# Performance work log

Measured on AMD Instinct MI355X. Metric: run time of the kernel, lower is better.

Reference implementation:

```python
import jax, jax.numpy as jnp
import numpy as np

B, C, H, W = 16, 128, 64, 64
L, ND = 512, 256
GROUPS = 32
EPS = 1e-6


def setup_inputs() -> dict:
    key = jax.random.key(0)
    ks = jax.random.split(key, 8)
    return {
        "x": jax.random.normal(ks[0], (B, C, H, W), dtype=jnp.float32),
        "nd": jax.random.normal(ks[1], (B, L, ND), dtype=jnp.float32),
        "gn_gamma": jnp.ones((C,), dtype=jnp.float32),
        "gn_beta": jnp.zeros((C,), dtype=jnp.float32),
        "q_w": jax.random.normal(ks[2], (C, C), dtype=jnp.float32) * 0.02,
        "q_b": jax.random.normal(ks[3], (C,), dtype=jnp.float32) * 0.02,
        "nd_w": jax.random.normal(ks[4], (C, ND), dtype=jnp.float32) * 0.02,
        "nd_b": jax.random.normal(ks[5], (C,), dtype=jnp.float32) * 0.02,
        "proj_w": jax.random.normal(ks[6], (C, C), dtype=jnp.float32) * 0.02,
        "proj_b": jax.random.normal(ks[7], (C,), dtype=jnp.float32) * 0.02,
    }


def _group_norm(x, gamma, beta):
    b, c, h, w = x.shape
    xr = x.reshape(b, GROUPS, c // GROUPS, h, w)
    mean = xr.mean(axis=(2, 3, 4), keepdims=True)
    var = xr.var(axis=(2, 3, 4), keepdims=True)
    xn = ((xr - mean) * jax.lax.rsqrt(var + EPS)).reshape(b, c, h, w)
    return xn * gamma[None, :, None, None] + beta[None, :, None, None]


def reference(x, nd, gn_gamma, gn_beta, q_w, q_b, nd_w, nd_b, proj_w, proj_b):
    b, c, h, w = x.shape
    hn = _group_norm(x, gn_gamma, gn_beta)
    # 1x1 conv query -> [b, hw, c]
    q = jnp.einsum('bchw,oc->bhwo', hn, q_w).reshape(b, h * w, c) + q_b
    # silu + linear projection of conditioning; k and v use identical projection/input
    kv = jax.nn.silu(nd) @ nd_w.T + nd_b  # [b, L, c]
    # attention: [b, hw, L]
    logits = jnp.einsum('bnc,blc->bnl', q, kv) * (c ** -0.5)
    attn = jax.nn.softmax(logits, axis=2)
    # weighted sum of v -> [b, c, hw] -> [b, c, h, w]
    out = jnp.einsum('blc,bnl->bcn', kv, attn).reshape(b, c, h, w)
    # 1x1 conv projection
    out = jnp.einsum('bchw,oc->bohw', out, proj_w) + proj_b[None, :, None, None]
    return x + out
```

## Files before the change

### kernel.cpp

```cpp
#include <hip/hip_runtime.h>
#include <math.h>

constexpr int kB = 16, kC = 128, kHW = 4096, kL = 512, kND = 256, kG = 32;
constexpr float kEps = 1e-6f;
constexpr float kScale = 0.08838834764831845f;

typedef short sv8 __attribute__((ext_vector_type(8)));
typedef int   iv4 __attribute__((ext_vector_type(4)));
typedef float f32x16 __attribute__((ext_vector_type(16)));

static __device__ __forceinline__ unsigned short f2bf(float f) {
    unsigned int u = __builtin_bit_cast(unsigned int, f);
    u += 0x7fffu + ((u >> 16) & 1u);
    return (unsigned short)(u >> 16);
}
static __device__ __forceinline__ float bf2f(unsigned short s) {
    unsigned int u = ((unsigned int)s) << 16;
    return __builtin_bit_cast(float, u);
}
static __device__ __forceinline__ unsigned int pack2(float a, float b) {
    return (unsigned int)f2bf(a) | ((unsigned int)f2bf(b) << 16);
}

#define GLOAD_LDS16(gp, lp)                                                     \
    __builtin_amdgcn_global_load_lds(                                           \
        (const __attribute__((address_space(1))) void*)(gp),                    \
        (__attribute__((address_space(3))) void*)(lp), 16, 0, 0)

__global__ __launch_bounds__(256) void prep_all_k(
    const float* __restrict__ x, const float* __restrict__ nd,
    const float* __restrict__ nd_w, const float* __restrict__ nd_b,
    const float* __restrict__ proj_w, const float* __restrict__ q_w,
    const float* __restrict__ gamma, const float* __restrict__ beta,
    float* __restrict__ gab, unsigned short* __restrict__ kv_bf,
    unsigned short* __restrict__ kvT_bf, unsigned short* __restrict__ pwb,
    unsigned short* __restrict__ qwb)
{
    __shared__ float s_lds[8][256];
    __shared__ float w_lds[128][68];
    __shared__ float t_lds[8][129];
    __shared__ float red8[8];
    const int bid = blockIdx.x;
    const int tid = threadIdx.x;

    if (bid < 512) {
        const float4* p4 = (const float4*)(x + (size_t)bid * 4 * kHW);
        float s = 0.f, ss = 0.f;
        for (int i = tid; i < 4096; i += 256) {
            float4 v = p4[i];
            s  += (v.x + v.y) + (v.z + v.w);
            ss += (v.x * v.x + v.y * v.y) + (v.z * v.z + v.w * v.w);
        }
#pragma unroll
        for (int off = 1; off < 64; off <<= 1) {
            s  += __shfl_xor(s, off, 64);
            ss += __shfl_xor(ss, off, 64);
        }
        int wid = tid >> 6;
        if ((tid & 63) == 0) { red8[wid] = s; red8[wid + 4] = ss; }
        __syncthreads();
        if (tid == 0) {
            float S  = (red8[0] + red8[1]) + (red8[2] + red8[3]);
            float SS = (red8[4] + red8[5]) + (red8[6] + red8[7]);
            float mean = S * (1.f / 16384.f);
            float var  = SS * (1.f / 16384.f) - mean * mean;
            red8[0] = mean;
            red8[1] = rsqrtf(var + kEps);
        }
        __syncthreads();
        if (tid < 4) {
            int bb = bid >> 5, g = bid & 31, c = g * 4 + tid;
            float mean = red8[0], rstd = red8[1];
            float ga = gamma[c] * rstd;
            gab[bb * 256 + c]       = ga;
            gab[bb * 256 + 128 + c] = beta[c] - mean * ga;
        }
        return;
    }
    if (bid >= 1536) {
        const float* src = (bid < 1552) ? proj_w : q_w;
        unsigned short* dst = (bid < 1552) ? pwb : qwb;
        int i = (((bid - 1536) & 15) * 256 + tid) * 4;
        float4 v = *(const float4*)(src + i);
        dst[i + 0] = f2bf(v.x); dst[i + 1] = f2bf(v.y);
        dst[i + 2] = f2bf(v.z); dst[i + 3] = f2bf(v.w);
        return;
    }
    {
        int idx0 = bid - 512;
        int b = idx0 >> 6;
        int l0 = (idx0 & 63) * 8;
        const float4* ndp = (const float4*)(nd + ((size_t)b * kL + l0) * kND);
#pragma unroll
        for (int r = 0; r < 2; r++) {
            int idx = tid + r * 256;
            int row = idx >> 6;
            int c4 = idx & 63;
            float4 v = ndp[row * 64 + c4];
            v.x = v.x / (1.f + __expf(-v.x));
            v.y = v.y / (1.f + __expf(-v.y));
            v.z = v.z / (1.f + __expf(-v.z));
            v.w = v.w / (1.f + __expf(-v.w));
            *(float4*)&s_lds[row][c4 * 4] = v;
        }
        float acc[4] = {0.f, 0.f, 0.f, 0.f};
        int lr = tid >> 5;
        int oq = tid & 31;
        for (int d0 = 0; d0 < kND; d0 += 64) {
            __syncthreads();
#pragma unroll
            for (int r = 0; r < 8; r++) {
                int idx = tid + r * 256;
                int row = idx >> 4;
                int c4 = idx & 15;
                float4 v = ((const float4*)(nd_w + (size_t)row * kND + d0))[c4];
                *(float4*)&w_lds[row][c4 * 4] = v;
            }
            __syncthreads();
            for (int dd = 0; dd < 64; dd += 4) {
                float4 sv = *(const float4*)&s_lds[lr][d0 + dd];
#pragma unroll
                for (int j = 0; j < 4; j++) {
                    float4 wv = *(const float4*)&w_lds[oq + 32 * j][dd];
                    acc[j] += sv.x * wv.x + sv.y * wv.y + sv.z * wv.z + sv.w * wv.w;
                }
            }
        }
#pragma unroll
        for (int j = 0; j < 4; j++) {
            int o = oq + 32 * j;
            float vout = acc[j] + nd_b[o];
            kv_bf[((size_t)b * kL + l0 + lr) * kC + o] = f2bf(vout);
            t_lds[lr][o] = vout;
        }
        __syncthreads();
        int o = tid >> 1, lh = (tid & 1) * 4;
        unsigned long long pk = 0;
#pragma unroll
        for (int i = 0; i < 4; i++)
            pk |= (unsigned long long)f2bf(t_lds[lh + i][o]) << (16 * i);
        *(unsigned long long*)(kvT_bf + ((size_t)b * kC + o) * kL + l0 + lh) = pk;
    }
}

__global__ __launch_bounds__(256, 2) void attn_k(
    const float* __restrict__ x,
    const float* __restrict__ gab,
    const float* __restrict__ q_b,
    const unsigned short* __restrict__ qwb,
    const unsigned short* __restrict__ kvb,
    const unsigned short* __restrict__ kvtb,
    const unsigned short* __restrict__ pwb,
    const float* __restrict__ proj_b,
    float* __restrict__ out)
{
    __shared__ __align__(16) char smem[51200];

    const int flat = blockIdx.y * gridDim.x + blockIdx.x;
    const int b  = ((flat & 7) << 1) | ((flat >> 3) & 1);
    const int n0 = (flat >> 4) * 128;
    const int tid = threadIdx.x;
    const int wave = tid >> 6;
    const int lane = tid & 63;
    const int lrow = lane & 31;
    const int hi = lane >> 5;
    const int swzA = (lrow & 15) << 4;
    const int swzT = ((lrow >> 1) & 3) << 4;

    float* x_lds = (float*)(smem + 32768);
    float* gtab  = (float*)(smem + 49152);

    const unsigned short* kvB  = kvb  + (size_t)b * kL * kC;
    const unsigned short* kvtB = kvtb + (size_t)b * kC * kL;

#define STAGE_TILE(tt) do {                                                     \
        int l0s = (tt) << 5;                                                    \
        char* dA = smem + (((tt) & 1) * 8192);                                  \
        char* dT = smem + 16384 + (((tt) & 1) * 8192);                          \
        _Pragma("unroll")                                                       \
        for (int i = 0; i < 2; i++) {                                           \
            int l = i * 16 + wave * 4 + (lane >> 4);                            \
            int ch = lane & 15;                                                 \
            const unsigned short* gs =                                          \
                kvB + (size_t)(l0s + l) * kC + ((ch ^ (l & 15)) * 8);           \
            GLOAD_LDS16(gs, dA + (i * 256 + wave * 64) * 16);                   \
        }                                                                       \
        _Pragma("unroll")                                                       \
        for (int i = 0; i < 2; i++) {                                           \
            int c = i * 64 + wave * 16 + (lane >> 2);                           \
            int ch = lane & 3;                                                  \
            const unsigned short* gs =                                          \
                kvtB + (size_t)c * kL + l0s + ((ch ^ ((c >> 1) & 3)) * 8);      \
            GLOAD_LDS16(gs, dT + (i * 256 + wave * 64) * 16);                   \
        }                                                                       \
    } while (0)

    STAGE_TILE(0);

    if (tid < 64)
        ((float4*)gtab)[tid] = ((const float4*)(gab + b * 256))[tid];
    else if (tid < 96)
        ((float4*)gtab)[tid] = ((const float4*)q_b)[tid - 64];
    __syncthreads();

    f32x16 dq[4];
#pragma unroll
    for (int ot = 0; ot < 4; ot++)
#pragma unroll
        for (int r = 0; r < 16; r++) dq[ot][r] = 0.f;

    for (int cc = 0; cc < 4; cc++) {
#pragma unroll
        for (int k = 0; k < 4; k++) {
            int idx = tid + k * 256;
            int c = idx >> 5, n4 = idx & 31;
            int cg = cc * 32 + c;
            float4 v = *(const float4*)(
                x + ((size_t)b * kC + cg) * kHW + n0 + n4 * 4);
            float ga = gtab[cg], be = gtab[128 + cg];
            v.x = v.x * ga + be; v.y = v.y * ga + be;
            v.z = v.z * ga + be; v.w = v.w * ga + be;
            *(float4*)&x_lds[c * 128 + n4 * 4] = v;
        }
        __syncthreads();
#pragma unroll
        for (int kk = 0; kk < 2; kk++) {
            sv8 bh;
#pragma unroll
            for (int j = 0; j < 8; j++)
                bh[j] = (short)f2bf(x_lds[(kk * 16 + hi * 8 + j) * 128 + wave * 32 + lrow]);
#pragma unroll
            for (int ot = 0; ot < 4; ot++) {
                const unsigned short* arow =
                    qwb + (size_t)(ot * 32 + lrow) * kC + cc * 32 + kk * 16 + hi * 8;
                dq[ot] = __builtin_amdgcn_mfma_f32_32x32x16_bf16(
                             *(const sv8*)arow, bh, dq[ot], 0, 0, 0);
            }
        }
        __syncthreads();
    }

    sv8 qa[8];
#pragma unroll
    for (int ot = 0; ot < 4; ot++) {
        unsigned int pk[4], pk2[4];
#pragma unroll
        for (int g = 0; g < 4; g++) {
            int ob = ot * 32 + 8 * g + 4 * hi;
            float4 qb4 = *(const float4*)&gtab[256 + ob];
            float v0 = (dq[ot][4 * g + 0] + qb4.x) * kScale;
            float v1 = (dq[ot][4 * g + 1] + qb4.y) * kScale;
            float v2 = (dq[ot][4 * g + 2] + qb4.z) * kScale;
            float v3 = (dq[ot][4 * g + 3] + qb4.w) * kScale;
            pk[g]  = pack2(v0, v1);
            pk2[g] = pack2(v2, v3);
        }
#pragma unroll
        for (int kk = 0; kk < 2; kk++) {
            unsigned int a_lo = pk[kk * 2],  a_hi = pk[kk * 2 + 1];
            unsigned int b_lo = pk2[kk * 2], b_hi = pk2[kk * 2 + 1];
            unsigned int own_a = hi ? a_hi : a_lo;
            unsigned int own_b = hi ? b_hi : b_lo;
            unsigned int rcv_a = (unsigned int)__shfl_xor((int)(hi ? a_lo : a_hi), 32, 64);
            unsigned int rcv_b = (unsigned int)__shfl_xor((int)(hi ? b_lo : b_hi), 32, 64);
            iv4 w;
            w[0] = (int)(hi ? rcv_a : own_a);
            w[1] = (int)(hi ? rcv_b : own_b);
            w[2] = (int)(hi ? own_a : rcv_a);
            w[3] = (int)(hi ? own_b : rcv_b);
            qa[2 * ot + kk] = __builtin_bit_cast(sv8, w);
        }
    }

    f32x16 oacc[4];
#pragma unroll
    for (int ct = 0; ct < 4; ct++)
#pragma unroll
        for (int r = 0; r < 16; r++) oacc[ct][r] = 0.f;
    float rsumv = 0.f;

    for (int t = 0; t < 16; t++) {
        const char* bufA = smem + (t & 1) * 8192;
        const char* bufT = smem + 16384 + (t & 1) * 8192;
        if (t < 15) STAGE_TILE(t + 1);

        f32x16 s;
#pragma unroll
        for (int r = 0; r < 16; r++) s[r] = 0.f;
        {
            const char* arow = bufA + lrow * 256;
            __builtin_amdgcn_s_setprio(1);
#pragma unroll
            for (int kc = 0; kc < 8; kc++)
                s = __builtin_amdgcn_mfma_f32_32x32x16_bf16(
                        *(const sv8*)(arow + ((kc * 32 + hi * 16) ^ swzA)),
                        qa[kc], s, 0, 0, 0);
            __builtin_amdgcn_s_setprio(0);
        }
        float p[16];
#pragma unroll
        for (int r = 0; r < 16; r++) {
            p[r] = __expf(s[r]);
            rsumv += p[r];
        }
        unsigned int pk[4], pk2[4];
#pragma unroll
        for (int g = 0; g < 4; g++) {
            pk[g]  = pack2(p[4 * g + 0], p[4 * g + 1]);
            pk2[g] = pack2(p[4 * g + 2], p[4 * g + 3]);
        }
        sv8 pv[2];
#pragma unroll
        for (int kk = 0; kk < 2; kk++) {
            unsigned int a_lo = pk[kk * 2],  a_hi = pk[kk * 2 + 1];
            unsigned int b_lo = pk2[kk * 2], b_hi = pk2[kk * 2 + 1];
            unsigned int own_a = hi ? a_hi : a_lo;
            unsigned int own_b = hi ? b_hi : b_lo;
            unsigned int rcv_a = (unsigned int)__shfl_xor((int)(hi ? a_lo : a_hi), 32, 64);
            unsigned int rcv_b = (unsigned int)__shfl_xor((int)(hi ? b_lo : b_hi), 32, 64);
            iv4 w;
            w[0] = (int)(hi ? rcv_a : own_a);
            w[1] = (int)(hi ? rcv_b : own_b);
            w[2] = (int)(hi ? own_a : rcv_a);
            w[3] = (int)(hi ? own_b : rcv_b);
            pv[kk] = __builtin_bit_cast(sv8, w);
        }
        __builtin_amdgcn_s_setprio(1);
#pragma unroll
        for (int ct = 0; ct < 4; ct++) {
            const char* rowp = bufT + (ct * 32 + lrow) * 64;
#pragma unroll
            for (int kk = 0; kk < 2; kk++)
                oacc[ct] = __builtin_amdgcn_mfma_f32_32x32x16_bf16(
                               pv[kk],
                               *(const sv8*)(rowp + ((kk * 32 + hi * 16) ^ swzT)),
                               oacc[ct], 0, 0, 0);
        }
        __builtin_amdgcn_s_setprio(0);

        __syncthreads();
    }

    float total = rsumv + __shfl_xor(rsumv, 32, 64);
    float* rs = (float*)(smem + 50688) + wave * 32;
    rs[lrow] = 1.0f / total;
    float rinv[16];
#pragma unroll
    for (int r = 0; r < 16; r++)
        rinv[r] = rs[(r & 3) + 8 * (r >> 2) + 4 * hi];

    unsigned short* o_lds = (unsigned short*)smem;
    __syncthreads();
#pragma unroll
    for (int ct = 0; ct < 4; ct++)
#pragma unroll
        for (int r = 0; r < 16; r++) {
            int n = wave * 32 + (r & 3) + 8 * (r >> 2) + 4 * hi;
            o_lds[n * 136 + ct * 32 + lrow] = f2bf(oacc[ct][r] * rinv[r]);
        }
    sv8 oa[8];
    {
        const unsigned short* orow = o_lds + (wave * 32 + lrow) * 136 + hi * 8;
#pragma unroll
        for (int kc = 0; kc < 8; kc++) oa[kc] = *(const sv8*)(orow + kc * 16);
    }
    f32x16 dacc[4];
#pragma unroll
    for (int ot = 0; ot < 4; ot++)
#pragma unroll
        for (int r = 0; r < 16; r++) dacc[ot][r] = 0.f;
#pragma unroll
    for (int ot = 0; ot < 4; ot++) {
        const unsigned short* brow = pwb + (ot * 32 + lrow) * kC + hi * 8;
#pragma unroll
        for (int kc = 0; kc < 8; kc++)
            dacc[ot] = __builtin_amdgcn_mfma_f32_32x32x16_bf16(
                           oa[kc], *(const sv8*)(brow + kc * 16), dacc[ot], 0, 0, 0);
    }
#pragma unroll
    for (int ot = 0; ot < 4; ot++)
#pragma unroll
        for (int r = 0; r < 16; r++) {
            int n = wave * 32 + (r & 3) + 8 * (r >> 2) + 4 * hi;
            o_lds[n * 136 + ot * 32 + lrow] = f2bf(dacc[ot][r]);
        }
    __syncthreads();
#pragma unroll 4
    for (int it = 0; it < 64; it++) {
        int idx = it * 256 + tid;
        int o = idx >> 7, n = idx & 127;
        size_t gi = ((size_t)b * kC + o) * kHW + n0 + n;
        out[gi] = bf2f(o_lds[n * 136 + o]) + proj_b[o] + x[gi];
    }
#undef STAGE_TILE
}

extern "C" void kernel_launch(void* const* d_in, const int* in_sizes, int n_in,
                              void* d_out, int out_size, void* d_ws, size_t ws_size,
                              hipStream_t stream) {
    const float* x      = (const float*)d_in[0];
    const float* nd     = (const float*)d_in[1];
    const float* gamma  = (const float*)d_in[2];
    const float* beta   = (const float*)d_in[3];
    const float* q_w    = (const float*)d_in[4];
    const float* q_b    = (const float*)d_in[5];
    const float* nd_w   = (const float*)d_in[6];
    const float* nd_b   = (const float*)d_in[7];
    const float* proj_w = (const float*)d_in[8];
    const float* proj_b = (const float*)d_in[9];
    float* out = (float*)d_out;

    float* gab             = (float*)d_ws;
    unsigned short* pwb    = (unsigned short*)(gab + 4096);
    unsigned short* qwb    = pwb + 16384;
    unsigned short* kv_bf  = qwb + 16384;
    unsigned short* kvT_bf = kv_bf + (size_t)kB * kL * kC;

    prep_all_k<<<dim3(1568), dim3(256), 0, stream>>>(
        x, nd, nd_w, nd_b, proj_w, q_w, gamma, beta, gab, kv_bf, kvT_bf, pwb, qwb);
    attn_k<<<dim3(kHW / 128, kB), dim3(256), 0, stream>>>(
        x, gab, q_b, qwb, kv_bf, kvT_bf, pwb, proj_b, out);
}
```

Baseline: 82.13 us.

## Halve attention tile to 64 positions, split channel tiles across wave pairs

The attention kernel now processes 64 spatial positions per block instead of 128, with waves paired so each pair shares a 32-row query group and splits the output channel tiles in half. This doubles the grid, shrinks LDS to about 34KB and raises launch bounds to 3 blocks per SM, aiming for better occupancy and load balance across CUs. The cost is that each K/V tile is now staged from global/L2 twice as often per output position, and the Q projection and softmax are computed redundantly by both waves of a pair. Extra barriers are also added around the shared output buffer.

Result: slower. 101.2 us (+23.3%).

```diff
diff --git a/kernel.cpp b/kernel.cpp
--- a/kernel.cpp
+++ b/kernel.cpp
@@ -143,7 +143,7 @@
     }
 }
 
-__global__ __launch_bounds__(256, 2) void attn_k(
+__global__ __launch_bounds__(256, 3) void attn_k(
     const float* __restrict__ x,
     const float* __restrict__ gab,
     const float* __restrict__ q_b,
@@ -154,21 +154,24 @@
     const float* __restrict__ proj_b,
     float* __restrict__ out)
 {
-    __shared__ __align__(16) char smem[51200];
-
-    const int flat = blockIdx.y * gridDim.x + blockIdx.x;
-    const int b  = ((flat & 7) << 1) | ((flat >> 3) & 1);
-    const int n0 = (flat >> 4) * 128;
+    __shared__ __align__(16) char smem[34816];
+
+    const int flat = blockIdx.x;
+    const int bg = flat & 15;
+    const int b  = ((bg & 7) << 1) | (bg >> 3);
+    const int n0 = (flat >> 4) * 64;
     const int tid = threadIdx.x;
     const int wave = tid >> 6;
+    const int rg = wave >> 1;
+    const int ch = wave & 1;
     const int lane = tid & 63;
     const int lrow = lane & 31;
     const int hi = lane >> 5;
     const int swzA = (lrow & 15) << 4;
     const int swzT = ((lrow >> 1) & 3) << 4;
 
-    float* x_lds = (float*)(smem + 32768);
-    float* gtab  = (float*)(smem + 49152);
+    float* x_lds = (float*)(smem + 8192);
+    float* gtab  = (float*)(smem + 32768);
 
     const unsigned short* kvB  = kvb  + (size_t)b * kL * kC;
     const unsigned short* kvtB = kvtb + (size_t)b * kC * kL;
@@ -180,17 +183,17 @@
         _Pragma("unroll")                                                       \
         for (int i = 0; i < 2; i++) {                                           \
             int l = i * 16 + wave * 4 + (lane >> 4);                            \
-            int ch = lane & 15;                                                 \
+            int c2 = lane & 15;                                                 \
             const unsigned short* gs =                                          \
-                kvB + (size_t)(l0s + l) * kC + ((ch ^ (l & 15)) * 8);           \
+                kvB + (size_t)(l0s + l) * kC + ((c2 ^ (l & 15)) * 8);           \
             GLOAD_LDS16(gs, dA + (i * 256 + wave * 64) * 16);                   \
         }                                                                       \
         _Pragma("unroll")                                                       \
         for (int i = 0; i < 2; i++) {                                           \
             int c = i * 64 + wave * 16 + (lane >> 2);                           \
-            int ch = lane & 3;                                                  \
+            int c2 = lane & 3;                                                  \
             const unsigned short* gs =                                          \
-                kvtB + (size_t)c * kL + l0s + ((ch ^ ((c >> 1) & 3)) * 8);      \
+                kvtB + (size_t)c * kL + l0s + ((c2 ^ ((c >> 1) & 3)) * 8);      \
             GLOAD_LDS16(gs, dT + (i * 256 + wave * 64) * 16);                   \
         }                                                                       \
     } while (0)
@@ -211,16 +214,16 @@
 
     for (int cc = 0; cc < 4; cc++) {
 #pragma unroll
-        for (int k = 0; k < 4; k++) {
+        for (int k = 0; k < 2; k++) {
             int idx = tid + k * 256;
-            int c = idx >> 5, n4 = idx & 31;
+            int c = idx >> 4, n4 = idx & 15;
             int cg = cc * 32 + c;
             float4 v = *(const float4*)(
                 x + ((size_t)b * kC + cg) * kHW + n0 + n4 * 4);
             float ga = gtab[cg], be = gtab[128 + cg];
             v.x = v.x * ga + be; v.y = v.y * ga + be;
             v.z = v.z * ga + be; v.w = v.w * ga + be;
-            *(float4*)&x_lds[c * 128 + n4 * 4] = v;
+            *(float4*)&x_lds[c * 64 + n4 * 4] = v;
         }
         __syncthreads();
 #pragma unroll
@@ -228,7 +231,7 @@
             sv8 bh;
 #pragma unroll
             for (int j = 0; j < 8; j++)
-                bh[j] = (short)f2bf(x_lds[(kk * 16 + hi * 8 + j) * 128 + wave * 32 + lrow]);
+                bh[j] = (short)f2bf(x_lds[(kk * 16 + hi * 8 + j) * 64 + rg * 32 + lrow]);
 #pragma unroll
             for (int ot = 0; ot < 4; ot++) {
                 const unsigned short* arow =
@@ -271,10 +274,11 @@
             qa[2 * ot + kk] = __builtin_bit_cast(sv8, w);
         }
     }
-
-    f32x16 oacc[4];
-#pragma unroll
-    for (int ct = 0; ct < 4; ct++)
+    __syncthreads();
+
+    f32x16 oacc[2];
+#pragma unroll
+    for (int ct = 0; ct < 2; ct++)
 #pragma unroll
         for (int r = 0; r < 16; r++) oacc[ct][r] = 0.f;
     float rsumv = 0.f;
@@ -327,14 +331,15 @@
         }
         __builtin_amdgcn_s_setprio(1);
 #pragma unroll
-        for (int ct = 0; ct < 4; ct++) {
+        for (int ctl = 0; ctl < 2; ctl++) {
+            int ct = ch * 2 + ctl;
             const char* rowp = bufT + (ct * 32 + lrow) * 64;
 #pragma unroll
             for (int kk = 0; kk < 2; kk++)
-                oacc[ct] = __builtin_amdgcn_mfma_f32_32x32x16_bf16(
+                oacc[ctl] = __builtin_amdgcn_mfma_f32_32x32x16_bf16(
                                pv[kk],
                                *(const sv8*)(rowp + ((kk * 32 + hi * 16) ^ swzT)),
-                               oacc[ct], 0, 0, 0);
+                               oacc[ctl], 0, 0, 0);
         }
         __builtin_amdgcn_s_setprio(0);
 
@@ -342,7 +347,7 @@
     }
 
     float total = rsumv + __shfl_xor(rsumv, 32, 64);
-    float* rs = (float*)(smem + 50688) + wave * 32;
+    float* rs = (float*)(smem + 34304) + wave * 32;
     rs[lrow] = 1.0f / total;
     float rinv[16];
 #pragma unroll
@@ -352,43 +357,50 @@
     unsigned short* o_lds = (unsigned short*)smem;
     __syncthreads();
 #pragma unroll
-    for (int ct = 0; ct < 4; ct++)
+    for (int ctl = 0; ctl < 2; ctl++) {
+        int ct = ch * 2 + ctl;
 #pragma unroll
         for (int r = 0; r < 16; r++) {
-            int n = wave * 32 + (r & 3) + 8 * (r >> 2) + 4 * hi;
-            o_lds[n * 136 + ct * 32 + lrow] = f2bf(oacc[ct][r] * rinv[r]);
-        }
+            int n = rg * 32 + (r & 3) + 8 * (r >> 2) + 4 * hi;
+            o_lds[n * 136 + ct * 32 + lrow] = f2bf(oacc[ctl][r] * rinv[r]);
+        }
+    }
+    __syncthreads();
     sv8 oa[8];
     {
-        const unsigned short* orow = o_lds + (wave * 32 + lrow) * 136 + hi * 8;
+        const unsigned short* orow = o_lds + (rg * 32 + lrow) * 136 + hi * 8;
 #pragma unroll
         for (int kc = 0; kc < 8; kc++) oa[kc] = *(const sv8*)(orow + kc * 16);
     }
-    f32x16 dacc[4];
-#pragma unroll
-    for (int ot = 0; ot < 4; ot++)
+    f32x16 dacc[2];
+#pragma unroll
+    for (int ot = 0; ot < 2; ot++)
 #pragma unroll
         for (int r = 0; r < 16; r++) dacc[ot][r] = 0.f;
 #pragma unroll
-    for (int ot = 0; ot < 4; ot++) {
+    for (int otl = 0; otl < 2; otl++) {
+        int ot = ch * 2 + otl;
         const unsigned short* brow = pwb + (ot * 32 + lrow) * kC + hi * 8;
 #pragma unroll
         for (int kc = 0; kc < 8; kc++)
-            dacc[ot] = __builtin_amdgcn_mfma_f32_32x32x16_bf16(
-                           oa[kc], *(const sv8*)(brow + kc * 16), dacc[ot], 0, 0, 0);
-    }
-#pragma unroll
-    for (int ot = 0; ot < 4; ot++)
+            dacc[otl] = __builtin_amdgcn_mfma_f32_32x32x16_bf16(
+                           oa[kc], *(const sv8*)(brow + kc * 16), dacc[otl], 0, 0, 0);
+    }
+    __syncthreads();
+#pragma unroll
+    for (int otl = 0; otl < 2; otl++) {
+        int ot = ch * 2 + otl;
 #pragma unroll
         for (int r = 0; r < 16; r++) {
-            int n = wave * 32 + (r & 3) + 8 * (r >> 2) + 4 * hi;
-            o_lds[n * 136 + ot * 32 + lrow] = f2bf(dacc[ot][r]);
-        }
+            int n = rg * 32 + (r & 3) + 8 * (r >> 2) + 4 * hi;
+            o_lds[n * 136 + ot * 32 + lrow] = f2bf(dacc[otl][r]);
+        }
+    }
     __syncthreads();
 #pragma unroll 4
-    for (int it = 0; it < 64; it++) {
+    for (int it = 0; it < 32; it++) {
         int idx = it * 256 + tid;
-        int o = idx >> 7, n = idx & 127;
+        int o = idx >> 6, n = idx & 63;
         size_t gi = ((size_t)b * kC + o) * kHW + n0 + n;
         out[gi] = bf2f(o_lds[n * 136 + o]) + proj_b[o] + x[gi];
     }
@@ -418,6 +430,6 @@
 
     prep_all_k<<<dim3(1568), dim3(256), 0, stream>>>(
         x, nd, nd_w, nd_b, proj_w, q_w, gamma, beta, gab, kv_bf, kvT_bf, pwb, qwb);
-    attn_k<<<dim3(kHW / 128, kB), dim3(256), 0, stream>>>(
+    attn_k<<<dim3(kHW / 64 * kB), dim3(256), 0, stream>>>(
         x, gab, q_b, qwb, kv_bf, kvT_bf, pwb, proj_b, out);
 }
```
